# Kernel tuning notes

Hardware: AMD Instinct MI355X
Metric: run time of the kernel (lower is better)

The kernel has to match this reference:

```python
import jax, jax.numpy as jnp
import numpy as np

S, B, H, V, U = 200, 1024, 128, 100000, 10000
LAMBDA_T = 0.1
LAMBDA_S = 1000.0
DAY = 86400.0


def setup_inputs() -> dict:
    key = jax.random.key(0)
    ks = jax.random.split(key, 14)
    x = jax.random.randint(ks[0], (S, B), 0, V)
    # monotone timestamps per sequence (gaps up to 1 hour)
    gaps = jax.random.uniform(ks[1], (S, B), minval=0.0, maxval=3600.0)
    t = jnp.cumsum(gaps, axis=0).astype(jnp.float32)
    # small spatial extent so exp(-1000*dist) doesn't fully underflow
    s = (jax.random.uniform(ks[2], (S, B, 2)) * 0.01).astype(jnp.float32)
    y_t = jax.random.uniform(ks[3], (S, B), dtype=jnp.float32)
    y_s = jax.random.uniform(ks[4], (S, B, 2), dtype=jnp.float32)
    h = jnp.zeros((B, H), dtype=jnp.float32)
    active_user = jax.random.randint(ks[5], (B,), 0, U)
    length = jax.random.randint(ks[6], (B,), 1, S + 1)
    W_enc = jax.random.normal(ks[7], (V, H), dtype=jnp.float32) * 0.02
    W_user = jax.random.normal(ks[8], (U, H), dtype=jnp.float32) * 0.02
    W_ih = jax.random.normal(ks[9], (H, H), dtype=jnp.float32) * 0.05
    W_hh = jax.random.normal(ks[10], (H, H), dtype=jnp.float32) * 0.05
    b_ih = jnp.zeros((H,), dtype=jnp.float32)
    b_hh = jnp.zeros((H,), dtype=jnp.float32)
    W_fc = jax.random.normal(ks[11], (V, 2 * H), dtype=jnp.float32) * 0.02
    b_fc = jnp.zeros((V,), dtype=jnp.float32)
    return {"x": x, "t": t, "s": s, "y_t": y_t, "y_s": y_s, "h": h,
            "active_user": active_user, "length": length,
            "W_enc": W_enc, "W_user": W_user, "W_ih": W_ih, "W_hh": W_hh,
            "b_ih": b_ih, "b_hh": b_hh, "W_fc": W_fc, "b_fc": b_fc}


def f_t(dt):
    return ((jnp.cos(dt * (2.0 * np.pi / DAY)) + 1.0) * 0.5) * jnp.exp(-(dt / DAY) * LAMBDA_T)


def f_s(ds):
    return jnp.exp(-ds * LAMBDA_S)


def reference(x, t, s, y_t, y_s, h, active_user, length,
              W_enc, W_user, W_ih, W_hh, b_ih, b_hh, W_fc, b_fc):
    seq_len, batch = x.shape
    x_emb = W_enc[x]  # [S,B,H]

    # vanilla tanh RNN over time (packing only affects padded steps, which are masked out below)
    def step(h_prev, x_t):
        h_new = jnp.tanh(x_t @ W_ih.T + b_ih + h_prev @ W_hh.T + b_hh)
        return h_new, h_new
    _, out = jax.lax.scan(step, h, x_emb)      # [S,B,H]
    out = out.transpose(1, 0, 2)               # [B,S,H]

    bidx = jnp.arange(batch)
    last = length - 1
    t_bt = t.T                                 # [B,S]
    s_bt = s.transpose(1, 0, 2)                # [B,S,2]
    t_last = t_bt[bidx, last]                  # [B]
    s_last = s_bt[bidx, last]                  # [B,2]

    dist_t = t_last[:, None] - t_bt                              # [B,S]
    dist_s = jnp.linalg.norm(s_last[:, None, :] - s_bt, axis=-1)  # [B,S]

    mask = jnp.arange(seq_len)[None, :] < length[:, None]        # [B,S] ragged mask
    w = jnp.where(mask, f_t(dist_t) * f_s(dist_s) + 1e-10, 0.0)  # [B,S]

    out_w = jnp.einsum('bs,bsh->bh', w, out) / jnp.sum(w, axis=1, keepdims=True)  # [B,H]

    p_u = W_user[active_user]                  # [B,H]
    out_pu = jnp.concatenate([out_w, p_u], axis=1)  # [B,2H]
    return out_pu @ W_fc.T + b_fc              # [B,V]
```

## Files before the change

### kernel.cpp

```cpp
#include <hip/hip_runtime.h>
#include <stdint.h>

#define S_LEN 200
#define BATCH 1024
#define HID   128
#define VOCAB 100000

typedef __attribute__((ext_vector_type(4))) float f32x4;
typedef __attribute__((ext_vector_type(8))) short bf16x8;

__device__ __forceinline__ unsigned short f2bf(float f) {
  union { float f; uint32_t u; } v; v.f = f;
  uint32_t u = v.u;
  uint32_t r = u + 0x7fffu + ((u >> 16) & 1u);
  return (unsigned short)(r >> 16);
}

__global__ __launch_bounds__(256) void k0_wfc_bf16(
    const float* __restrict__ Wfc, unsigned short* __restrict__ Wfcb) {
  size_t i = ((size_t)blockIdx.x * 256 + threadIdx.x) * 8;
  f32x4 a = *(const f32x4*)&Wfc[i];
  f32x4 b = *(const f32x4*)&Wfc[i + 4];
  uint4 pk;
  pk.x = (uint32_t)f2bf(a.x) | ((uint32_t)f2bf(a.y) << 16);
  pk.y = (uint32_t)f2bf(a.z) | ((uint32_t)f2bf(a.w) << 16);
  pk.z = (uint32_t)f2bf(b.x) | ((uint32_t)f2bf(b.y) << 16);
  pk.w = (uint32_t)f2bf(b.z) | ((uint32_t)f2bf(b.w) << 16);
  *(uint4*)&Wfcb[i] = pk;
}

__global__ __launch_bounds__(256) void k1_eprecomp(
    const float* __restrict__ Wenc, const float* __restrict__ Wih,
    const float* __restrict__ bih, const float* __restrict__ bhh,
    float* __restrict__ E) {
  __shared__ float Wlds[128][132];
  __shared__ float Alds[64][132];
  const int tid = threadIdx.x;
  const int v0 = blockIdx.x * 64;

  #pragma unroll
  for (int i = 0; i < 16; ++i) {
    int g = tid + i * 256;
    int row = g >> 5, c4 = g & 31;
    *(f32x4*)&Wlds[row][c4 * 4] = *(const f32x4*)&Wih[row * 128 + c4 * 4];
  }
  #pragma unroll
  for (int i = 0; i < 8; ++i) {
    int g = tid + i * 256;
    int row = g >> 5, c4 = g & 31;
    int v = v0 + row;
    *(f32x4*)&Alds[row][c4 * 4] =
        *(const f32x4*)&Wenc[(size_t)(v < VOCAB ? v : 0) * 128 + c4 * 4];
  }
  __syncthreads();

  const int jt = tid & 15, vt = tid >> 4;
  float acc[4][8];
  #pragma unroll
  for (int a = 0; a < 4; ++a)
    #pragma unroll
    for (int b = 0; b < 8; ++b) acc[a][b] = 0.f;

  for (int kk = 0; kk < 32; ++kk) {
    f32x4 av[4], wv[8];
    #pragma unroll
    for (int vv = 0; vv < 4; ++vv) av[vv] = *(const f32x4*)&Alds[vt + 16 * vv][kk * 4];
    #pragma unroll
    for (int jj = 0; jj < 8; ++jj) wv[jj] = *(const f32x4*)&Wlds[jt + 16 * jj][kk * 4];
    #pragma unroll
    for (int vv = 0; vv < 4; ++vv)
      #pragma unroll
      for (int jj = 0; jj < 8; ++jj)
        acc[vv][jj] += av[vv].x * wv[jj].x + av[vv].y * wv[jj].y +
                       av[vv].z * wv[jj].z + av[vv].w * wv[jj].w;
  }

  #pragma unroll
  for (int jj = 0; jj < 8; ++jj) {
    int j = jt + 16 * jj;
    float bias = bih[j] + bhh[j];
    #pragma unroll
    for (int vv = 0; vv < 4; ++vv) {
      int v = v0 + vt + 16 * vv;
      if (v < VOCAB) E[(size_t)v * 128 + j] = acc[vv][jj] + bias;
    }
  }
}

__global__ __launch_bounds__(256) void k1b_weights(
    const float* __restrict__ t, const float* __restrict__ s,
    const int* __restrict__ length, float* __restrict__ wbuf) {
  int idx = blockIdx.x * 256 + threadIdx.x;
  int ts = idx >> 10, b = idx & 1023;
  int len = length[b];
  float w = 0.f;
  if (ts < len) {
    int last = len - 1;
    float tl  = t[last * BATCH + b];
    float slx = s[(last * BATCH + b) * 2 + 0];
    float sly = s[(last * BATCH + b) * 2 + 1];
    float dt = tl - t[ts * BATCH + b];
    float dx = slx - s[(ts * BATCH + b) * 2 + 0];
    float dy = sly - s[(ts * BATCH + b) * 2 + 1];
    float ds = sqrtf(dx * dx + dy * dy);
    float ft = (__cosf(dt * 7.2722052166430399e-05f) + 1.f) * 0.5f *
               __expf(dt * -1.1574074074074073e-06f);
    float fs = __expf(-1000.f * ds);
    w = ft * fs + 1e-10f;
  }
  wbuf[idx] = w;
}

__global__ __launch_bounds__(256) void k2_rnn(
    const int* __restrict__ x, const float* __restrict__ E,
    const float* __restrict__ Whh, const float* __restrict__ h0,
    const float* __restrict__ wbuf,
    const int* __restrict__ active_user, const float* __restrict__ Wuser,
    unsigned short* __restrict__ A) {
  __shared__ float hlds[2][2][128];
  const int tid = threadIdx.x;
  const int lane = tid & 63, wv = tid >> 6;
  const int j = wv * 32 + (lane >> 1);
  const int kh = lane & 1;
  const int b0 = blockIdx.x * 2, b1 = b0 + 1;

  f32x4 Wr[16];
  const float* wrow = &Whh[j * 128 + kh * 64];
  #pragma unroll
  for (int i = 0; i < 16; ++i) Wr[i] = *(const f32x4*)&wrow[i * 4];

  { int bb = tid >> 7, jj = tid & 127;
    hlds[0][bb][jj] = h0[(b0 + bb) * 128 + jj]; }
  __syncthreads();

  float acc0 = 0.f, acc1 = 0.f, ws0 = 0.f, ws1 = 0.f;
  int xc0 = x[b0], xc1 = x[b1];
  int xn0 = x[1024 + b0], xn1 = x[1024 + b1];
  float ec0 = E[(size_t)xc0 * 128 + j], ec1 = E[(size_t)xc1 * 128 + j];
  float wc0 = wbuf[b0], wc1 = wbuf[b1];

  for (int t = 0; t < S_LEN; ++t) {
    int rb = t & 1, wb = rb ^ 1;
    int xf0 = 0, xf1 = 0;
    float en0 = 0.f, en1 = 0.f, wn0 = 0.f, wn1 = 0.f;
    if (t + 2 < S_LEN) { xf0 = x[(t + 2) * 1024 + b0]; xf1 = x[(t + 2) * 1024 + b1]; }
    if (t + 1 < S_LEN) {
      en0 = E[(size_t)xn0 * 128 + j]; en1 = E[(size_t)xn1 * 128 + j];
      wn0 = wbuf[(t + 1) * 1024 + b0]; wn1 = wbuf[(t + 1) * 1024 + b1];
    }
    float p0 = 0.f, p1 = 0.f;
    const float* h0p = &hlds[rb][0][kh * 64];
    const float* h1p = &hlds[rb][1][kh * 64];
    #pragma unroll
    for (int i = 0; i < 16; ++i) {
      f32x4 hv0 = *(const f32x4*)&h0p[i * 4];
      f32x4 hv1 = *(const f32x4*)&h1p[i * 4];
      p0 += Wr[i].x * hv0.x + Wr[i].y * hv0.y + Wr[i].z * hv0.z + Wr[i].w * hv0.w;
      p1 += Wr[i].x * hv1.x + Wr[i].y * hv1.y + Wr[i].z * hv1.z + Wr[i].w * hv1.w;
    }
    p0 += __shfl_xor(p0, 1, 64);
    p1 += __shfl_xor(p1, 1, 64);
    float hn0 = tanhf(p0 + ec0);
    float hn1 = tanhf(p1 + ec1);
    acc0 += wc0 * hn0; ws0 += wc0;
    acc1 += wc1 * hn1; ws1 += wc1;
    if (kh == 0) { hlds[wb][0][j] = hn0; hlds[wb][1][j] = hn1; }
    __syncthreads();
    xc0 = xn0; xc1 = xn1; xn0 = xf0; xn1 = xf1;
    ec0 = en0; ec1 = en1; wc0 = wn0; wc1 = wn1;
  }

  if (kh == 0) {
    A[b0 * 256 + j] = f2bf(acc0 / ws0);
    A[b1 * 256 + j] = f2bf(acc1 / ws1);
    int u0 = active_user[b0], u1 = active_user[b1];
    A[b0 * 256 + 128 + j] = f2bf(Wuser[u0 * 128 + j]);
    A[b1 * 256 + 128 + j] = f2bf(Wuser[u1 * 128 + j]);
  }
}

template <bool PRE>
__global__ __launch_bounds__(256) void k3_gemm(
    const unsigned short* __restrict__ Ab, const void* __restrict__ W,
    const float* __restrict__ bfc, float* __restrict__ out) {
  __shared__ unsigned short Alds[64 * 256];
  const int tid = threadIdx.x;
  const int bid = blockIdx.x;
  const int linear = (bid & 7) * 782 + (bid >> 3);
  const int nblk = linear >> 4;
  const int mblk = linear & 15;
  const int m0 = mblk * 64;
  const int v0 = nblk * 256;

  #pragma unroll
  for (int i = 0; i < 8; ++i) {
    int u = tid + i * 256;
    int row = u >> 5, cu = u & 31;
    uint32_t byte = (uint32_t)(row << 9) + (uint32_t)(cu << 4);
    byte ^= (uint32_t)((row & 7) << 4);
    uint4 val = *(const uint4*)&Ab[(size_t)(m0 + row) * 256 + cu * 8];
    *(uint4*)((char*)Alds + byte) = val;
  }
  __syncthreads();

  const int lane = tid & 63, wid = tid >> 6;
  const int lm = lane & 15, quad = lane >> 4;
  const int vbase = v0 + wid * 64;

  f32x4 acc[4][4];
  #pragma unroll
  for (int mt = 0; mt < 4; ++mt)
    #pragma unroll
    for (int nt = 0; nt < 4; ++nt) acc[mt][nt] = (f32x4){0.f, 0.f, 0.f, 0.f};

  const char* bbase[4];
  #pragma unroll
  for (int nt = 0; nt < 4; ++nt) {
    int v = vbase + nt * 16 + lm;
    size_t vc = (size_t)(v < VOCAB ? v : (VOCAB - 1));
    if constexpr (PRE)
      bbase[nt] = (const char*)((const unsigned short*)W + vc * 256);
    else
      bbase[nt] = (const char*)((const float*)W + vc * 256);
  }

  for (int kc = 0; kc < 8; ++kc) {
    const int k0 = kc * 32 + quad * 8;
    bf16x8 af[4], bfr[4];
    #pragma unroll
    for (int mt = 0; mt < 4; ++mt) {
      int row = mt * 16 + lm;
      uint32_t byte = (uint32_t)(row << 9) + (uint32_t)(k0 << 1);
      byte ^= (uint32_t)((row & 7) << 4);
      af[mt] = *(const bf16x8*)((const char*)Alds + byte);
    }
    #pragma unroll
    for (int nt = 0; nt < 4; ++nt) {
      if constexpr (PRE) {
        bfr[nt] = *(const bf16x8*)(bbase[nt] + (size_t)k0 * 2);
      } else {
        const float* bp = (const float*)bbase[nt];
        f32x4 w0 = *(const f32x4*)&bp[k0];
        f32x4 w1 = *(const f32x4*)&bp[k0 + 4];
        bf16x8 b;
        b[0] = (short)f2bf(w0.x); b[1] = (short)f2bf(w0.y);
        b[2] = (short)f2bf(w0.z); b[3] = (short)f2bf(w0.w);
        b[4] = (short)f2bf(w1.x); b[5] = (short)f2bf(w1.y);
        b[6] = (short)f2bf(w1.z); b[7] = (short)f2bf(w1.w);
        bfr[nt] = b;
      }
    }
    #pragma unroll
    for (int mt = 0; mt < 4; ++mt)
      #pragma unroll
      for (int nt = 0; nt < 4; ++nt)
        acc[mt][nt] = __builtin_amdgcn_mfma_f32_16x16x32_bf16(
            af[mt], bfr[nt], acc[mt][nt], 0, 0, 0);
  }

  #pragma unroll
  for (int nt = 0; nt < 4; ++nt) {
    int v = vbase + nt * 16 + lm;
    if (v >= VOCAB) continue;
    float bias = bfc[v];
    #pragma unroll
    for (int mt = 0; mt < 4; ++mt) {
      int row = m0 + mt * 16 + quad * 4;
      #pragma unroll
      for (int r = 0; r < 4; ++r)
        out[(size_t)(row + r) * VOCAB + v] = acc[mt][nt][r] + bias;
    }
  }
}

extern "C" void kernel_launch(void* const* d_in, const int* in_sizes, int n_in,
                              void* d_out, int out_size, void* d_ws, size_t ws_size,
                              hipStream_t stream) {
  const int*   x     = (const int*)d_in[0];
  const float* t     = (const float*)d_in[1];
  const float* s     = (const float*)d_in[2];
  const float* h0    = (const float*)d_in[5];
  const int*   au    = (const int*)d_in[6];
  const int*   len   = (const int*)d_in[7];
  const float* Wenc  = (const float*)d_in[8];
  const float* Wuser = (const float*)d_in[9];
  const float* Wih   = (const float*)d_in[10];
  const float* Whh   = (const float*)d_in[11];
  const float* bih   = (const float*)d_in[12];
  const float* bhh   = (const float*)d_in[13];
  const float* Wfc   = (const float*)d_in[14];
  const float* bfc   = (const float*)d_in[15];
  float* out = (float*)d_out;

  char* ws = (char*)d_ws;
  float*          E    = (float*)(ws);
  float*          wbuf = (float*)(ws + 51200000);
  unsigned short* Ab   = (unsigned short*)(ws + 52019200);
  unsigned short* Wfcb = (unsigned short*)(ws + 52543488);
  const size_t need = 52543488ull + 51200000ull;
  const bool pre = ws_size >= need;

  if (pre) k0_wfc_bf16<<<12500, 256, 0, stream>>>(Wfc, Wfcb);
  k1_eprecomp<<<1563, 256, 0, stream>>>(Wenc, Wih, bih, bhh, E);
  k1b_weights<<<800, 256, 0, stream>>>(t, s, len, wbuf);
  k2_rnn<<<512, 256, 0, stream>>>(x, E, Whh, h0, wbuf, au, Wuser, Ab);
  if (pre)
    k3_gemm<true><<<6256, 256, 0, stream>>>(Ab, (const void*)Wfcb, bfc, out);
  else
    k3_gemm<false><<<6256, 256, 0, stream>>>(Ab, (const void*)Wfc, bfc, out);
}
```

Before: 1.027 ms.

## Run RNN with one batch row per block, padded LDS and fast tanh

The recurrent kernel now gives each block one sequence instead of two, which doubles the grid to 1024 blocks, and sets a launch bound of 4 blocks per SM. The hidden-state LDS buffer is padded so the two k-halves land in different banks, the dot product accumulates into vector lanes, and tanhf is replaced by an exp-based approximation. The aim is to shorten the serial per-step critical path and raise occupancy on the latency-bound scan. The cost is that each W_hh register tile now serves only one sequence, so weight-load work per sequence doubles. The fast tanh may also lose accuracy or overflow for large inputs.

```diff
diff --git a/kernel.cpp b/kernel.cpp
--- a/kernel.cpp
+++ b/kernel.cpp
@@ -14,6 +14,11 @@
   uint32_t u = v.u;
   uint32_t r = u + 0x7fffu + ((u >> 16) & 1u);
   return (unsigned short)(r >> 16);
+}
+
+__device__ __forceinline__ float tanh_fast(float x) {
+  float e = __expf(2.0f * x);
+  return 1.0f - 2.0f / (e + 1.0f);
 }
 
 __global__ __launch_bounds__(256) void k0_wfc_bf16(
@@ -111,71 +116,62 @@
   wbuf[idx] = w;
 }
 
-__global__ __launch_bounds__(256) void k2_rnn(
+__global__ __launch_bounds__(256, 4) void k2_rnn(
     const int* __restrict__ x, const float* __restrict__ E,
     const float* __restrict__ Whh, const float* __restrict__ h0,
     const float* __restrict__ wbuf,
     const int* __restrict__ active_user, const float* __restrict__ Wuser,
     unsigned short* __restrict__ A) {
-  __shared__ float hlds[2][2][128];
+  __shared__ float hlds[2][144];
   const int tid = threadIdx.x;
   const int lane = tid & 63, wv = tid >> 6;
   const int j = wv * 32 + (lane >> 1);
   const int kh = lane & 1;
-  const int b0 = blockIdx.x * 2, b1 = b0 + 1;
+  const int b = blockIdx.x;
 
   f32x4 Wr[16];
   const float* wrow = &Whh[j * 128 + kh * 64];
   #pragma unroll
   for (int i = 0; i < 16; ++i) Wr[i] = *(const f32x4*)&wrow[i * 4];
 
-  { int bb = tid >> 7, jj = tid & 127;
-    hlds[0][bb][jj] = h0[(b0 + bb) * 128 + jj]; }
+  if (tid < 128) hlds[0][tid + (tid >> 6) * 8] = h0[b * 128 + tid];
   __syncthreads();
 
-  float acc0 = 0.f, acc1 = 0.f, ws0 = 0.f, ws1 = 0.f;
-  int xc0 = x[b0], xc1 = x[b1];
-  int xn0 = x[1024 + b0], xn1 = x[1024 + b1];
-  float ec0 = E[(size_t)xc0 * 128 + j], ec1 = E[(size_t)xc1 * 128 + j];
-  float wc0 = wbuf[b0], wc1 = wbuf[b1];
+  float acc = 0.f, ws = 0.f;
+  int xc = x[b];
+  int xn = x[1024 + b];
+  float ec = E[(size_t)xc * 128 + j];
+  float wc = wbuf[b];
 
   for (int t = 0; t < S_LEN; ++t) {
     int rb = t & 1, wb = rb ^ 1;
-    int xf0 = 0, xf1 = 0;
-    float en0 = 0.f, en1 = 0.f, wn0 = 0.f, wn1 = 0.f;
-    if (t + 2 < S_LEN) { xf0 = x[(t + 2) * 1024 + b0]; xf1 = x[(t + 2) * 1024 + b1]; }
+    int xf = 0;
+    float en = 0.f, wn = 0.f;
+    if (t + 2 < S_LEN) xf = x[(t + 2) * 1024 + b];
     if (t + 1 < S_LEN) {
-      en0 = E[(size_t)xn0 * 128 + j]; en1 = E[(size_t)xn1 * 128 + j];
-      wn0 = wbuf[(t + 1) * 1024 + b0]; wn1 = wbuf[(t + 1) * 1024 + b1];
-    }
-    float p0 = 0.f, p1 = 0.f;
-    const float* h0p = &hlds[rb][0][kh * 64];
-    const float* h1p = &hlds[rb][1][kh * 64];
+      en = E[(size_t)xn * 128 + j];
+      wn = wbuf[(t + 1) * 1024 + b];
+    }
+    const float* hp = &hlds[rb][kh * 72];
+    f32x4 a4 = (f32x4){0.f, 0.f, 0.f, 0.f};
     #pragma unroll
     for (int i = 0; i < 16; ++i) {
-      f32x4 hv0 = *(const f32x4*)&h0p[i * 4];
-      f32x4 hv1 = *(const f32x4*)&h1p[i * 4];
-      p0 += Wr[i].x * hv0.x + Wr[i].y * hv0.y + Wr[i].z * hv0.z + Wr[i].w * hv0.w;
-      p1 += Wr[i].x * hv1.x + Wr[i].y * hv1.y + Wr[i].z * hv1.z + Wr[i].w * hv1.w;
-    }
-    p0 += __shfl_xor(p0, 1, 64);
-    p1 += __shfl_xor(p1, 1, 64);
-    float hn0 = tanhf(p0 + ec0);
-    float hn1 = tanhf(p1 + ec1);
-    acc0 += wc0 * hn0; ws0 += wc0;
-    acc1 += wc1 * hn1; ws1 += wc1;
-    if (kh == 0) { hlds[wb][0][j] = hn0; hlds[wb][1][j] = hn1; }
+      f32x4 hv = *(const f32x4*)&hp[i * 4];
+      a4 += Wr[i] * hv;
+    }
+    float p = (a4.x + a4.y) + (a4.z + a4.w);
+    p += __shfl_xor(p, 1, 64);
+    float hn = tanh_fast(p + ec);
+    acc += wc * hn; ws += wc;
+    if (kh == 0) hlds[wb][j + (j >> 6) * 8] = hn;
     __syncthreads();
-    xc0 = xn0; xc1 = xn1; xn0 = xf0; xn1 = xf1;
-    ec0 = en0; ec1 = en1; wc0 = wn0; wc1 = wn1;
+    xc = xn; xn = xf; ec = en; wc = wn;
   }
 
   if (kh == 0) {
-    A[b0 * 256 + j] = f2bf(acc0 / ws0);
-    A[b1 * 256 + j] = f2bf(acc1 / ws1);
-    int u0 = active_user[b0], u1 = active_user[b1];
-    A[b0 * 256 + 128 + j] = f2bf(Wuser[u0 * 128 + j]);
-    A[b1 * 256 + 128 + j] = f2bf(Wuser[u1 * 128 + j]);
+    A[b * 256 + j] = f2bf(acc / ws);
+    int u = active_user[b];
+    A[b * 256 + 128 + j] = f2bf(Wuser[u * 128 + j]);
   }
 }
 
@@ -303,7 +299,7 @@
   if (pre) k0_wfc_bf16<<<12500, 256, 0, stream>>>(Wfc, Wfcb);
   k1_eprecomp<<<1563, 256, 0, stream>>>(Wenc, Wih, bih, bhh, E);
   k1b_weights<<<800, 256, 0, stream>>>(t, s, len, wbuf);
-  k2_rnn<<<512, 256, 0, stream>>>(x, E, Whh, h0, wbuf, au, Wuser, Ab);
+  k2_rnn<<<1024, 256, 0, stream>>>(x, E, Whh, h0, wbuf, au, Wuser, Ab);
   if (pre)
     k3_gemm<true><<<6256, 256, 0, stream>>>(Ab, (const void*)Wfcb, bfc, out);
   else
```

New measurement: 927.6 us. -9.7%, faster.
